# Kernel optimization log

Measured on AMD Instinct MI355X. Metric: run time of the kernel, lower is better.

Reference implementation:

```python
import jax, jax.numpy as jnp
import numpy as np


def setup_inputs() -> dict:
    key = jax.random.key(0)
    k1, k2, k3 = jax.random.split(key, 3)
    B, T, D = 16, 2048, 256
    input_feature = jax.random.normal(k1, (B, T, 2 * D), dtype=jnp.float32)
    W = jax.random.normal(k2, (D, D), dtype=jnp.float32) * 0.05
    b = jax.random.normal(k3, (D,), dtype=jnp.float32) * 0.05
    return {"input_feature": input_feature, "W": W, "b": b}


def reference(input_feature, W, b):
    # chunk into two halves along last dim and sum -> h: [B, T, 256]
    h1, h2 = jnp.split(input_feature, 2, axis=-1)
    h = h1 + h2
    # attention_layer: Linear(256,256) + ReLU  (torch Linear: x @ W.T + b)
    atten_w = jax.nn.relu(jnp.einsum('btd,ed->bte', h, W) + b)  # [B, T, 256]
    m = jnp.tanh(h)
    # bmm(m, atten_w^T): scores [B, T, T]
    atten_context = jnp.einsum('btd,bsd->bts', m, atten_w)
    softmax_w = jax.nn.softmax(atten_context, axis=-1)
    # bmm(h^T, softmax_w): [B, 256, T]
    context = jnp.einsum('btd,bts->bds', h, softmax_w)
    # residual add with h^T
    return jnp.swapaxes(h, 1, 2) + context
```

## Files before the change

kernel.cpp:

```cpp
#include <hip/hip_runtime.h>
#include <hip/hip_bf16.h>
#include <math.h>


#define NB 16
#define NT 2048
#define ND 256

typedef __attribute__((ext_vector_type(4))) float f32x4;
typedef __attribute__((ext_vector_type(8))) short s16x8;
typedef __attribute__((ext_vector_type(4))) short s16x4;
typedef __attribute__((ext_vector_type(8))) _Float16 f16x8;
typedef unsigned short u16;

__device__ __forceinline__ u16 f2h(float x) {
  union { _Float16 h; u16 u; } v; v.h = (_Float16)x; return v.u;
}
__device__ __forceinline__ float h2f(u16 u) {
  union { u16 u; _Float16 h; } v; v.u = u; return (float)v.h;
}
__device__ __forceinline__ float tanh_fast(float x) {
  return 1.f - 2.f / (1.f + __expf(2.f * x));
}
__device__ __forceinline__ void ldsbar() {
  __builtin_amdgcn_sched_barrier(0);
  asm volatile("s_waitcnt lgkmcnt(0)" ::: "memory");
  __builtin_amdgcn_s_barrier();
  __builtin_amdgcn_sched_barrier(0);
}

__global__ __launch_bounds__(256, 8) void kA(const float* __restrict__ inF,
    u16* __restrict__ h16, u16* __restrict__ m16, u16* __restrict__ hfrag)
{
  __shared__ __attribute__((aligned(16))) u16 hld[32][264];
  const int blk = blockIdx.x;
  const int b   = blk >> 6;
  const int t0  = (blk & 63) << 5;
  const int tid = threadIdx.x;
  const int w    = tid >> 6;
  const int lane = tid & 63;
  const int rh   = lane >> 5;
  const int dseg = (lane & 31) << 3;
  #pragma unroll
  for (int it = 0; it < 4; ++it) {
    const int rloc = w * 8 + it * 2 + rh;
    const size_t grow = (size_t)(b * NT + t0 + rloc);
    const float* base = inF + grow * (2 * ND) + dseg;
    float4 a0 = *(const float4*)(base);
    float4 a1 = *(const float4*)(base + 4);
    float4 c0 = *(const float4*)(base + ND);
    float4 c1 = *(const float4*)(base + ND + 4);
    float hv[8] = {a0.x + c0.x, a0.y + c0.y, a0.z + c0.z, a0.w + c0.w,
                   a1.x + c1.x, a1.y + c1.y, a1.z + c1.z, a1.w + c1.w};
    s16x8 vh, vm;
    #pragma unroll
    for (int r = 0; r < 8; ++r) {
      vh[r] = (short)f2h(hv[r]);
      vm[r] = (short)f2h(tanh_fast(hv[r]));
    }
    *(s16x8*)&hld[rloc][dseg] = vh;
    __builtin_nontemporal_store(vh, (s16x8*)(h16 + grow * ND + dseg));
    __builtin_nontemporal_store(vm, (s16x8*)(m16 + grow * ND + dseg));
  }
  ldsbar();
  u16* Hb = hfrag + (size_t)b * ND * NT;
  const int ti = t0 >> 5;
  #pragma unroll
  for (int s = 0; s < 4; ++s) {
    const int slot  = tid * 4 + s;
    const int dtile = slot >> 6;
    const int lp    = slot & 63;
    const int d  = dtile * 16 + (lp & 15);
    const int tb = (lp >> 4) * 8;
    s16x8 v;
    #pragma unroll
    for (int j = 0; j < 8; ++j) v[j] = (short)hld[tb + j][d];
    __builtin_nontemporal_store(v,
        (s16x8*)(Hb + (((size_t)dtile * (NT / 32) + ti) * 64 + lp) * 8));
  }
}

__global__ __launch_bounds__(256, 2) void kB(const u16* __restrict__ h16,
    const float* __restrict__ W, const float* __restrict__ bias, u16* __restrict__ aw16)
{
  __shared__ __attribute__((aligned(16))) u16 Wl[128][264];
  const int r0 = blockIdx.x << 7;
  const int e0 = blockIdx.y << 7;
  const int tid = threadIdx.x;
  #pragma unroll
  for (int rep = 0; rep < 16; ++rep) {
    const int idx = rep * 2048 + tid * 8;
    const int er = idx >> 8, col = idx & 255;
    float4 x0 = *(const float4*)(W + (size_t)(e0 + er) * ND + col);
    float4 x1 = *(const float4*)(W + (size_t)(e0 + er) * ND + col + 4);
    s16x8 v;
    v[0] = (short)f2h(x0.x); v[1] = (short)f2h(x0.y); v[2] = (short)f2h(x0.z); v[3] = (short)f2h(x0.w);
    v[4] = (short)f2h(x1.x); v[5] = (short)f2h(x1.y); v[6] = (short)f2h(x1.z); v[7] = (short)f2h(x1.w);
    *(s16x8*)&Wl[er][col] = v;
  }
  const int lane = tid & 63;
  const int w    = tid >> 6;
  const int l15  = lane & 15, kg = lane >> 4;
  float bv[8];
  #pragma unroll
  for (int et = 0; et < 8; ++et) bv[et] = bias[e0 + et * 16 + l15];
  f32x4 acc[2][8];
  #pragma unroll
  for (int rt = 0; rt < 2; ++rt)
    #pragma unroll
    for (int et = 0; et < 8; ++et) acc[rt][et] = (f32x4){0.f, 0.f, 0.f, 0.f};
  ldsbar();
  #pragma unroll
  for (int ks = 0; ks < 8; ++ks) {
    f16x8 af[2];
    #pragma unroll
    for (int rt = 0; rt < 2; ++rt)
      af[rt] = *(const f16x8*)(h16 + (size_t)(r0 + w * 32 + rt * 16 + l15) * ND + ks * 32 + kg * 8);
    #pragma unroll
    for (int et = 0; et < 8; ++et) {
      f16x8 bf = *(const f16x8*)&Wl[et * 16 + l15][ks * 32 + kg * 8];
      #pragma unroll
      for (int rt = 0; rt < 2; ++rt)
        acc[rt][et] = __builtin_amdgcn_mfma_f32_16x16x32_f16(af[rt], bf, acc[rt][et], 0, 0, 0);
    }
  }
  ldsbar();
  u16 (*awt)[132] = (u16 (*)[132])(&Wl[0][0]);
  #pragma unroll
  for (int rt = 0; rt < 2; ++rt)
    #pragma unroll
    for (int et = 0; et < 8; ++et) {
      const int e_loc = et * 16 + l15;
      #pragma unroll
      for (int r = 0; r < 4; ++r) {
        const int row_loc = w * 32 + rt * 16 + kg * 4 + r;
        float v = acc[rt][et][r] + bv[et];
        awt[row_loc][e_loc] = f2h(v > 0.f ? v : 0.f);
      }
    }
  ldsbar();
  #pragma unroll
  for (int it = 0; it < 8; ++it) {
    const int rloc = it * 16 + w * 4 + (lane >> 4);
    const int sb   = (lane & 15) << 3;
    s16x8 v = *(const s16x8*)&awt[rloc][sb];
    __builtin_nontemporal_store(v, (s16x8*)(aw16 + (size_t)(r0 + rloc) * ND + e0 + sb));
  }
}

__global__ __launch_bounds__(512, 4) void k2z(
    const u16* __restrict__ m16, const u16* __restrict__ aw16,
    u16* __restrict__ Sfrag, float* __restrict__ Zarr)
{
  __shared__ __attribute__((aligned(16))) u16 awch[2][64][264];
  __shared__ float zp[2][64];
  const int tt  = blockIdx.x;
  const int b   = blockIdx.y;
  const int t0  = tt << 6;
  const int tid = threadIdx.x;
  const int lane = tid & 63;
  const int w    = tid >> 6;
  const int grp  = w >> 2;
  const int wl   = w & 3;
  const int l15 = lane & 15, kg = lane >> 4;
  f16x8 afr[8];
  const size_t abase = ((size_t)(b * NT + t0 + wl * 16 + l15)) * ND + kg * 8;
  #pragma unroll
  for (int ks = 0; ks < 8; ++ks) afr[ks] = *(const f16x8*)(m16 + abase + ks * 32);
  const u16* awb = aw16 + (size_t)b * NT * ND;
  u16* STb = Sfrag + (size_t)b * NT * NT;
  const int ti    = tt * 2 + (wl >> 1);
  const int lanep = l15 + 16 * ((wl & 1) * 2 + (kg >> 1));
  const int jp    = (kg & 1) * 4;
  s16x8 rg[4];
  auto loadReg = [&](int step) {
    const int s0 = step << 6;
    #pragma unroll
    for (int rep = 0; rep < 4; ++rep) {
      const int idx = rep * 4096 + tid * 8;
      rg[rep] = *(const s16x8*)(awb + (size_t)(s0 + (idx >> 8)) * ND + (idx & 255));
    }
  };
  auto writeReg = [&](int buf) {
    #pragma unroll
    for (int rep = 0; rep < 4; ++rep) {
      const int idx = rep * 4096 + tid * 8;
      *(s16x8*)&awch[buf][idx >> 8][idx & 255] = rg[rep];
    }
  };
  loadReg(0); writeReg(0);
  loadReg(1);
  float zacc[4] = {0.f, 0.f, 0.f, 0.f};
  ldsbar();
  for (int step = 0; step < 32; ++step) {
    const int c = step & 1;
    if (step < 31) writeReg(c ^ 1);
    if (step < 30) loadReg(step + 2);
    f32x4 accS[2];
    accS[0] = (f32x4){0.f, 0.f, 0.f, 0.f};
    accS[1] = (f32x4){0.f, 0.f, 0.f, 0.f};
    __builtin_amdgcn_s_setprio(1);
    #pragma unroll
    for (int ks = 0; ks < 8; ++ks) {
      #pragma unroll
      for (int st = 0; st < 2; ++st) {
        f16x8 bf = *(const f16x8*)&awch[c][grp * 32 + st * 16 + l15][ks * 32 + kg * 8];
        accS[st] = __builtin_amdgcn_mfma_f32_16x16x32_f16(afr[ks], bf, accS[st], 0, 0, 0);
      }
    }
    __builtin_amdgcn_s_setprio(0);
    #pragma unroll
    for (int st = 0; st < 2; ++st) {
      const int si = step * 4 + grp * 2 + st;
      s16x4 sv;
      #pragma unroll
      for (int r = 0; r < 4; ++r) sv[r] = (short)f2h(accS[st][r]);
      *(s16x4*)(STb + (((size_t)si * 64 + ti) * 64 + lanep) * 8 + jp) = sv;
      #pragma unroll
      for (int r = 0; r < 4; ++r) zacc[r] += __expf(accS[st][r]);
    }
    ldsbar();
  }
  #pragma unroll
  for (int r = 0; r < 4; ++r) {
    #pragma unroll
    for (int o = 1; o < 16; o <<= 1) zacc[r] += __shfl_xor(zacc[r], o, 64);
  }
  if (l15 == 0) {
    #pragma unroll
    for (int r = 0; r < 4; ++r) zp[grp][wl * 16 + kg * 4 + r] = zacc[r];
  }
  ldsbar();
  if (tid < 64)
    Zarr[(size_t)b * NT + t0 + tid] = zp[0][tid] + zp[1][tid];
}

__global__ __launch_bounds__(512, 4) void k3o(
    const u16* __restrict__ Sfrag, const u16* __restrict__ hfrag,
    const float* __restrict__ Zarr, float* __restrict__ outp)
{
  __shared__ __attribute__((aligned(16))) u16 Pbuf[2][4][2][64][8];
  __shared__ float zld[NT];
  const int b   = blockIdx.y;
  const int s0t = blockIdx.x;
  const int tid = threadIdx.x;
  const int lane = tid & 63;
  const int w    = tid >> 6;
  const int l15 = lane & 15, kg = lane >> 4;
  const u16* Sb = Sfrag + (size_t)b * NT * NT;
  const u16* Hb = hfrag + (size_t)b * ND * NT;
  {
    float4 z = *(const float4*)(Zarr + (size_t)b * NT + tid * 4);
    zld[tid * 4 + 0] = 1.f / z.x;
    zld[tid * 4 + 1] = 1.f / z.y;
    zld[tid * 4 + 2] = 1.f / z.z;
    zld[tid * 4 + 3] = 1.f / z.w;
  }
  const int mst = w >> 1, mks = w & 1;
  const u16* sp = Sb + ((((size_t)(s0t * 4 + mst)) * 64 + mks) * 64 + lane) * 8;
  auto loadS = [&](int ch) -> s16x8 {
    return *(const s16x8*)(sp + (size_t)ch * 1024);
  };
  auto expP = [&](s16x8 v, int ch) -> s16x8 {
    const float* rzp = &zld[(ch * 2 + mks) * 32 + kg * 8];
    float4 ra = *(const float4*)rzp;
    float4 rb = *(const float4*)(rzp + 4);
    const float rv[8] = {ra.x, ra.y, ra.z, ra.w, rb.x, rb.y, rb.z, rb.w};
    s16x8 p;
    #pragma unroll
    for (int j = 0; j < 8; ++j) p[j] = (short)f2h(__expf(h2f((u16)v[j])) * rv[j]);
    return p;
  };
  auto loadH = [&](f16x8 (&dst)[2][2], int ch) {
    #pragma unroll
    for (int dt = 0; dt < 2; ++dt)
      #pragma unroll
      for (int ks = 0; ks < 2; ++ks)
        dst[dt][ks] = *(const f16x8*)(Hb + (((size_t)(w * 2 + dt) * 64 + ch * 2 + ks) * 64 + lane) * 8);
  };

  f32x4 acc[4][2];
  #pragma unroll
  for (int st = 0; st < 4; ++st) {
    acc[st][0] = (f32x4){0.f, 0.f, 0.f, 0.f};
    acc[st][1] = (f32x4){0.f, 0.f, 0.f, 0.f};
  }
  auto mfmaStep = [&](int cur, f16x8 (&hb)[2][2]) {
    __builtin_amdgcn_s_setprio(1);
    #pragma unroll
    for (int ks = 0; ks < 2; ++ks) {
      f16x8 pa[4];
      #pragma unroll
      for (int st = 0; st < 4; ++st)
        pa[st] = *(const f16x8*)&Pbuf[cur][st][ks][lane][0];
      #pragma unroll
      for (int dt = 0; dt < 2; ++dt)
        #pragma unroll
        for (int st = 0; st < 4; ++st)
          acc[st][dt] = __builtin_amdgcn_mfma_f32_16x16x32_f16(pa[st], hb[dt][ks], acc[st][dt], 0, 0, 0);
    }
    __builtin_amdgcn_s_setprio(0);
  };

  s16x8 d0 = loadS(0);
  s16x8 d1 = loadS(1);
  s16x8 d2 = loadS(2);
  f16x8 hA[2][2], hB[2][2];
  loadH(hA, 0);
  ldsbar();
  {
    s16x8 pr = expP(d0, 0);
    *(s16x8*)&Pbuf[0][mst][mks][lane][0] = pr;
  }
  ldsbar();

  for (int ch = 0; ch < 32; ch += 2) {
    loadH(hB, ch + 1);
    {
      s16x8 prn = expP(d1, ch + 1);
      d1 = d2;
      if (ch + 3 < 32) d2 = loadS(ch + 3);
      mfmaStep(0, hA);
      *(s16x8*)&Pbuf[1][mst][mks][lane][0] = prn;
    }
    ldsbar();
    if (ch + 2 < 32) loadH(hA, ch + 2);
    const bool wr = (ch + 2 < 32);
    s16x8 prn2;
    if (wr) prn2 = expP(d1, ch + 2);
    d1 = d2;
    if (ch + 4 < 32) d2 = loadS(ch + 4);
    mfmaStep(1, hB);
    if (wr) *(s16x8*)&Pbuf[0][mst][mks][lane][0] = prn2;
    ldsbar();
  }
  #pragma unroll
  for (int st = 0; st < 4; ++st) {
    const int sb = s0t * 64 + st * 16 + kg * 4;
    #pragma unroll
    for (int dt = 0; dt < 2; ++dt) {
      const int d = w * 32 + dt * 16 + l15;
      const u16* hres = Hb + (((size_t)(w * 2 + dt) * 64 + (s0t * 2 + (st >> 1))) * 64
                        + (l15 + 16 * ((st & 1) * 2 + (kg >> 1)))) * 8 + (kg & 1) * 4;
      float4 o;
      o.x = acc[st][dt][0] + h2f(hres[0]);
      o.y = acc[st][dt][1] + h2f(hres[1]);
      o.z = acc[st][dt][2] + h2f(hres[2]);
      o.w = acc[st][dt][3] + h2f(hres[3]);
      *(float4*)(outp + ((size_t)(b * ND + d)) * NT + sb) = o;
    }
  }
}

extern "C" void kernel_launch(void* const* d_in, const int* in_sizes, int n_in,
                              void* d_out, int out_size, void* d_ws, size_t ws_size,
                              hipStream_t stream) {
  const float* inF  = (const float*)d_in[0];
  const float* W    = (const float*)d_in[1];
  const float* bias = (const float*)d_in[2];
  float* outp = (float*)d_out;

  const size_t SZ = (size_t)NB * NT * ND;
  u16* m16   = (u16*)d_ws;
  u16* hfrag = m16 + SZ;
  u16* aw16  = hfrag + SZ;
  float* Zarr = (float*)(aw16 + SZ);
  u16* Sfrag = (u16*)(Zarr + (size_t)NB * NT);
  u16* h16   = Sfrag;
  const size_t need = 3 * SZ * sizeof(u16) + (size_t)NB * NT * sizeof(float)
                    + (size_t)NB * NT * NT * sizeof(u16);
  if (ws_size < need) return;

  kA <<<dim3(NB * NT / 32), dim3(256), 0, stream>>>(inF, h16, m16, hfrag);
  kB <<<dim3(256, 2), dim3(256), 0, stream>>>(h16, W, bias, aw16);
  k2z<<<dim3(32, NB), dim3(512), 0, stream>>>(m16, aw16, Sfrag, Zarr);
  k3o<<<dim3(NT / 64, NB), dim3(512), 0, stream>>>(Sfrag, hfrag, Zarr, outp);
}
```

Measured before the change: 170.3 us.

## Split k2z score pass over two key halves with separate Z reduction kernel

```diff
diff --git a/kernel.cpp b/kernel.cpp
--- a/kernel.cpp
+++ b/kernel.cpp
@@ -148,14 +148,15 @@
   }
 }
 
-__global__ __launch_bounds__(512, 4) void k2z(
+__global__ __launch_bounds__(512, 8) void k2z(
     const u16* __restrict__ m16, const u16* __restrict__ aw16,
-    u16* __restrict__ Sfrag, float* __restrict__ Zarr)
-{
-  __shared__ __attribute__((aligned(16))) u16 awch[2][64][264];
+    u16* __restrict__ Sfrag, float* __restrict__ Zpart)
+{
+  __shared__ __attribute__((aligned(16))) u16 awch[64][264];
   __shared__ float zp[2][64];
   const int tt  = blockIdx.x;
-  const int b   = blockIdx.y;
+  const int sh  = blockIdx.y;
+  const int b   = blockIdx.z;
   const int t0  = tt << 6;
   const int tid = threadIdx.x;
   const int lane = tid & 63;
@@ -174,28 +175,27 @@
   const int jp    = (kg & 1) * 4;
   s16x8 rg[4];
   auto loadReg = [&](int step) {
-    const int s0 = step << 6;
+    const int s0 = sh * (NT / 2) + (step << 6);
     #pragma unroll
     for (int rep = 0; rep < 4; ++rep) {
       const int idx = rep * 4096 + tid * 8;
       rg[rep] = *(const s16x8*)(awb + (size_t)(s0 + (idx >> 8)) * ND + (idx & 255));
     }
   };
-  auto writeReg = [&](int buf) {
+  auto writeReg = [&]() {
     #pragma unroll
     for (int rep = 0; rep < 4; ++rep) {
       const int idx = rep * 4096 + tid * 8;
-      *(s16x8*)&awch[buf][idx >> 8][idx & 255] = rg[rep];
-    }
-  };
-  loadReg(0); writeReg(0);
-  loadReg(1);
+      *(s16x8*)&awch[idx >> 8][idx & 255] = rg[rep];
+    }
+  };
+  loadReg(0);
   float zacc[4] = {0.f, 0.f, 0.f, 0.f};
-  ldsbar();
-  for (int step = 0; step < 32; ++step) {
-    const int c = step & 1;
-    if (step < 31) writeReg(c ^ 1);
-    if (step < 30) loadReg(step + 2);
+  for (int step = 0; step < 16; ++step) {
+    ldsbar();
+    writeReg();
+    if (step < 15) loadReg(step + 1);
+    ldsbar();
     f32x4 accS[2];
     accS[0] = (f32x4){0.f, 0.f, 0.f, 0.f};
     accS[1] = (f32x4){0.f, 0.f, 0.f, 0.f};
@@ -204,14 +204,14 @@
     for (int ks = 0; ks < 8; ++ks) {
       #pragma unroll
       for (int st = 0; st < 2; ++st) {
-        f16x8 bf = *(const f16x8*)&awch[c][grp * 32 + st * 16 + l15][ks * 32 + kg * 8];
+        f16x8 bf = *(const f16x8*)&awch[grp * 32 + st * 16 + l15][ks * 32 + kg * 8];
         accS[st] = __builtin_amdgcn_mfma_f32_16x16x32_f16(afr[ks], bf, accS[st], 0, 0, 0);
       }
     }
     __builtin_amdgcn_s_setprio(0);
     #pragma unroll
     for (int st = 0; st < 2; ++st) {
-      const int si = step * 4 + grp * 2 + st;
+      const int si = sh * 64 + step * 4 + grp * 2 + st;
       s16x4 sv;
       #pragma unroll
       for (int r = 0; r < 4; ++r) sv[r] = (short)f2h(accS[st][r]);
@@ -219,8 +219,8 @@
       #pragma unroll
       for (int r = 0; r < 4; ++r) zacc[r] += __expf(accS[st][r]);
     }
-    ldsbar();
-  }
+  }
+  ldsbar();
   #pragma unroll
   for (int r = 0; r < 4; ++r) {
     #pragma unroll
@@ -232,7 +232,16 @@
   }
   ldsbar();
   if (tid < 64)
-    Zarr[(size_t)b * NT + t0 + tid] = zp[0][tid] + zp[1][tid];
+    Zpart[((size_t)b * 2 + sh) * NT + t0 + tid] = zp[0][tid] + zp[1][tid];
+}
+
+__global__ __launch_bounds__(256) void kRed(const float* __restrict__ Zpart,
+    float* __restrict__ Zarr)
+{
+  const int b = blockIdx.y;
+  const int t = blockIdx.x * 256 + threadIdx.x;
+  Zarr[(size_t)b * NT + t] = Zpart[((size_t)b * 2 + 0) * NT + t]
+                           + Zpart[((size_t)b * 2 + 1) * NT + t];
 }
 
 __global__ __launch_bounds__(512, 4) void k3o(
@@ -367,12 +376,14 @@
   float* Zarr = (float*)(aw16 + SZ);
   u16* Sfrag = (u16*)(Zarr + (size_t)NB * NT);
   u16* h16   = Sfrag;
+  float* Zpart = outp;
   const size_t need = 3 * SZ * sizeof(u16) + (size_t)NB * NT * sizeof(float)
                     + (size_t)NB * NT * NT * sizeof(u16);
   if (ws_size < need) return;
 
-  kA <<<dim3(NB * NT / 32), dim3(256), 0, stream>>>(inF, h16, m16, hfrag);
-  kB <<<dim3(256, 2), dim3(256), 0, stream>>>(h16, W, bias, aw16);
-  k2z<<<dim3(32, NB), dim3(512), 0, stream>>>(m16, aw16, Sfrag, Zarr);
-  k3o<<<dim3(NT / 64, NB), dim3(512), 0, stream>>>(Sfrag, hfrag, Zarr, outp);
-}
+  kA  <<<dim3(NB * NT / 32), dim3(256), 0, stream>>>(inF, h16, m16, hfrag);
+  kB  <<<dim3(256, 2), dim3(256), 0, stream>>>(h16, W, bias, aw16);
+  k2z <<<dim3(32, 2, NB), dim3(512), 0, stream>>>(m16, aw16, Sfrag, Zpart);
+  kRed<<<dim3(NT / 256, NB), dim3(256), 0, stream>>>(Zpart, Zarr);
+  k3o <<<dim3(NT / 64, NB), dim3(512), 0, stream>>>(Sfrag, hfrag, Zarr, outp);
+}
```

After: 256.8 us. 50.8% more time.
